# Performance work log

Measured on AMD Instinct MI355X. Metric: run time of the kernel, lower is better.

Reference implementation:

```python
import jax, jax.numpy as jnp
import numpy as np

K = 16  # neighbors


def knn(x, k):
    # x: [B,N,C]; returns indices of k nearest points (incl. self) [B,N,k]
    sq = jnp.sum(x * x, axis=-1)
    d = sq[:, :, None] + sq[:, None, :] - 2.0 * jnp.einsum('bnc,bmc->bnm', x, x)
    return jax.lax.top_k(-d, k)[1]


def gather_nbrs(x, idx):
    # x: [B,N,C], idx: [B,N,k] -> [B,N,k,C]
    return jax.vmap(lambda xb, ib: xb[ib])(x, idx)


def bn(x, g, b, m, v):
    # Keras BatchNormalization inference mode, eps=1e-3
    return (x - m) * g * jax.lax.rsqrt(v + 1e-3) + b


def dense(x, w, b):
    # Conv1D(kernel_size=1) == pointwise dense over channels
    return jnp.einsum('bnc,co->bno', x, w) + b


def graph_layer(h, k, lw, lb, cw, cb, relu_out):
    g = gather_nbrs(h, knn(h, k))          # [B,N,k,C]
    m = jnp.max(g, axis=2)                 # [B,N,C] max over neighbors
    m = dense(dense(m, lw, lb), cw, cb)
    return jax.nn.relu(m) if relu_out else m


def setup_inputs():
    key = jax.random.key(0)
    ks = jax.random.split(key, 16)
    B, N = 16, 2048
    inp = {'x': jax.random.normal(ks[0], (B, N, 3), jnp.float32)}
    dims = [('conv1', 12, 12), ('conv2', 12, 64), ('conv3', 64, 64),
            ('g1_lin', 64, 64), ('g1_conv', 64, 128),
            ('g2_lin', 128, 128), ('g2_conv', 128, 1024),
            ('conv4', 1024, 1024), ('conv5', 1024, 512)]
    for j, (name, i, o) in enumerate(dims):
        s = (2.0 / (i + o)) ** 0.5  # glorot-ish
        inp[name + '_w'] = jax.random.normal(ks[j + 1], (i, o), jnp.float32) * s
        inp[name + '_b'] = jnp.zeros((o,), jnp.float32)
    for name, c in [('bn1', 12), ('bn2', 64), ('bn3', 64)]:
        inp[name + '_g'] = jnp.ones((c,), jnp.float32)
        inp[name + '_b'] = jnp.zeros((c,), jnp.float32)
        inp[name + '_m'] = jnp.zeros((c,), jnp.float32)
        inp[name + '_v'] = jnp.ones((c,), jnp.float32)
    return inp


def reference(x, conv1_w, conv1_b, conv2_w, conv2_b, conv3_w, conv3_b,
              g1_lin_w, g1_lin_b, g1_conv_w, g1_conv_b,
              g2_lin_w, g2_lin_b, g2_conv_w, g2_conv_b,
              conv4_w, conv4_b, conv5_w, conv5_b,
              bn1_g, bn1_b, bn1_m, bn1_v,
              bn2_g, bn2_b, bn2_m, bn2_v,
              bn3_g, bn3_b, bn3_m, bn3_v):
    B, N = x.shape[0], x.shape[1]
    kx = gather_nbrs(x, knn(x, K))                        # [B,N,K,3]
    c = kx - jnp.mean(kx, axis=2, keepdims=True)
    cov = jnp.einsum('bnki,bnkj->bnij', c, c)             # [B,N,3,3]
    h = jnp.concatenate([x, cov.reshape(B, N, 9)], axis=2)  # [B,N,12]
    h = jax.nn.relu(bn(dense(h, conv1_w, conv1_b), bn1_g, bn1_b, bn1_m, bn1_v))
    h = jax.nn.relu(bn(dense(h, conv2_w, conv2_b), bn2_g, bn2_b, bn2_m, bn2_v))
    h = jax.nn.relu(bn(dense(h, conv3_w, conv3_b), bn3_g, bn3_b, bn3_m, bn3_v))
    h = graph_layer(h, K, g1_lin_w, g1_lin_b, g1_conv_w, g1_conv_b, True)    # [B,N,128]
    h = graph_layer(h, K, g2_lin_w, g2_lin_b, g2_conv_w, g2_conv_b, False)   # [B,N,1024]
    h = jnp.max(h, axis=1, keepdims=True)                 # [B,1,1024]
    h = jax.nn.relu(dense(h, conv4_w, conv4_b))
    return dense(h, conv5_w, conv5_b)                     # [B,1,512]
```

## Files before the change

### kernel.cpp

```cpp
#include <hip/hip_runtime.h>
#include <cstddef>
#include <cstdint>

#define NPTS 2048

typedef short bf16x8 __attribute__((ext_vector_type(8)));
typedef float f32x4 __attribute__((ext_vector_type(4)));

__device__ __forceinline__ unsigned short f2bf(float f) {
  unsigned u = __builtin_bit_cast(unsigned, f);
  unsigned r = u + 0x7fffu + ((u >> 16) & 1u);
  return (unsigned short)(r >> 16);
}
__device__ __forceinline__ float bf2f(unsigned short s) {
  unsigned u = ((unsigned)s) << 16;
  return __builtin_bit_cast(float, u);
}
__device__ __forceinline__ unsigned f2sort(float f) {
  unsigned u = __builtin_bit_cast(unsigned, f);
  return u ^ (unsigned)(((int)u >> 31) | 0x80000000);
}

__device__ __forceinline__ void pool_insert(uint64_t k, uint64_t& s0, uint64_t& s1,
                                            uint64_t& s2, uint64_t& s3) {
  s3 = k < s3 ? k : s3;
  uint64_t t;
  t = s2 < s3 ? s2 : s3; s3 = s2 < s3 ? s3 : s2; s2 = t;
  t = s1 < s2 ? s1 : s2; s2 = s1 < s2 ? s2 : s1; s1 = t;
  t = s0 < s1 ? s0 : s1; s1 = s0 < s1 ? s1 : s0; s0 = t;
}

__device__ __forceinline__ int mbcnt64(unsigned long long m) {
  return __builtin_amdgcn_mbcnt_hi((unsigned)(m >> 32),
                                   __builtin_amdgcn_mbcnt_lo((unsigned)m, 0));
}

__device__ __forceinline__ float wave_sum_f32(float v) {
#pragma unroll
  for (int s = 1; s < 64; s <<= 1) v += __shfl_xor(v, s, 64);
  return v;
}

__global__ __launch_bounds__(256) void k_knn1_cov(const float* __restrict__ x,
                                                  float* __restrict__ h0) {
  const int b = blockIdx.y;
  const int tid = threadIdx.x;
  const int lane = tid & 63;
  const int w = tid >> 6;
  __shared__ float4 xsq[NPTS];
  const float* xb = x + (size_t)b * NPTS * 3;
  for (int i = tid; i < NPTS; i += 256) {
    float a0 = xb[3 * i], a1 = xb[3 * i + 1], a2 = xb[3 * i + 2];
    xsq[i] = make_float4(a0, a1, a2, fmaf(a0, a0, fmaf(a1, a1, a2 * a2)));
  }
  __syncthreads();
  const int nq = blockIdx.x * 4 + w;
  const float4 q4 = xsq[nq];
  const float sqq = q4.w;
  float d[32];
  uint64_t s0 = ~0ull, s1 = ~0ull, s2 = ~0ull, s3 = ~0ull;
#pragma unroll
  for (int j = 0; j < 32; ++j) {
    float4 v = xsq[j * 64 + lane];
    float dot = q4.x * v.x;
    dot = fmaf(q4.y, v.y, dot);
    dot = fmaf(q4.z, v.z, dot);
    float dd = fmaf(-2.f, dot, sqq + v.w);
    d[j] = dd;
    uint64_t k = ((uint64_t)f2sort(dd) << 32) | (unsigned)(j * 64 + lane);
    pool_insert(k, s0, s1, s2, s3);
  }
  const unsigned h0w = (unsigned)(s0 >> 32), m0i = (unsigned)s0;
  const unsigned h1w = (unsigned)(s1 >> 32), m1i = (unsigned)s1;
  const unsigned h2w = (unsigned)(s2 >> 32), m2i = (unsigned)s2;
  const unsigned h3w = (unsigned)(s3 >> 32), m3i = (unsigned)s3;
  unsigned H = 0;
#pragma unroll 1
  for (int bit = 31; bit >= 0; --bit) {
    unsigned tr = H | (1u << bit);
    int c = __popcll(__ballot(h0w < tr)) + __popcll(__ballot(h1w < tr)) +
            __popcll(__ballot(h2w < tr)) + __popcll(__ballot(h3w < tr));
    if (c < 16) H = tr;
  }
  const int cs = __popcll(__ballot(h0w < H)) + __popcll(__ballot(h1w < H)) +
                 __popcll(__ballot(h2w < H)) + __popcll(__ballot(h3w < H));
  const int rneed = 16 - cs;
  const bool e0 = (h0w == H), e1 = (h1w == H), e2 = (h2w == H), e3 = (h3w == H);
  const int gsz = __popcll(__ballot(e0)) + __popcll(__ballot(e1)) +
                  __popcll(__ballot(e2)) + __popcll(__ballot(e3));
  unsigned I = 0xFFFFFFFFu;
  if (gsz > rneed) {
    unsigned Iv = 0;
#pragma unroll 1
    for (int bit = 10; bit >= 0; --bit) {
      unsigned tr = Iv | (1u << bit);
      int c2 = __popcll(__ballot(e0 && m0i < tr)) + __popcll(__ballot(e1 && m1i < tr)) +
               __popcll(__ballot(e2 && m2i < tr)) + __popcll(__ballot(e3 && m3i < tr));
      if (c2 < rneed) Iv = tr;
    }
    I = Iv;
  }
  const bool sel0 = (h0w < H) | (e0 & (m0i <= I));
  const bool sel1 = (h1w < H) | (e1 & (m1i <= I));
  const bool sel2 = (h2w < H) | (e2 & (m2i <= I));
  const bool sel3 = (h3w < H) | (e3 & (m3i <= I));
  const int nsel = (int)sel0 + sel1 + sel2 + sel3;
  float cxx, cxy, cxz, cyy, cyz, czz;
  if (__ballot(nsel == 4) == 0ull) {
    float4 z = make_float4(0.f, 0.f, 0.f, 0.f);
    float4 v0 = sel0 ? xsq[m0i] : z;
    float4 v1 = sel1 ? xsq[m1i] : z;
    float4 v2 = sel2 ? xsq[m2i] : z;
    float4 v3 = sel3 ? xsq[m3i] : z;
    float sx = wave_sum_f32(v0.x + v1.x + v2.x + v3.x);
    float sy = wave_sum_f32(v0.y + v1.y + v2.y + v3.y);
    float sz = wave_sum_f32(v0.z + v1.z + v2.z + v3.z);
    const float mx = sx * 0.0625f, my = sy * 0.0625f, mz = sz * 0.0625f;
    float w0 = sel0 ? 1.f : 0.f, w1 = sel1 ? 1.f : 0.f;
    float w2 = sel2 ? 1.f : 0.f, w3 = sel3 ? 1.f : 0.f;
    float a0x = v0.x - mx, a0y = v0.y - my, a0z = v0.z - mz;
    float a1x = v1.x - mx, a1y = v1.y - my, a1z = v1.z - mz;
    float a2x = v2.x - mx, a2y = v2.y - my, a2z = v2.z - mz;
    float a3x = v3.x - mx, a3y = v3.y - my, a3z = v3.z - mz;
    float pxx = (w0 * a0x) * a0x + (w1 * a1x) * a1x + (w2 * a2x) * a2x + (w3 * a3x) * a3x;
    float pxy = (w0 * a0x) * a0y + (w1 * a1x) * a1y + (w2 * a2x) * a2y + (w3 * a3x) * a3y;
    float pxz = (w0 * a0x) * a0z + (w1 * a1x) * a1z + (w2 * a2x) * a2z + (w3 * a3x) * a3z;
    float pyy = (w0 * a0y) * a0y + (w1 * a1y) * a1y + (w2 * a2y) * a2y + (w3 * a3y) * a3y;
    float pyz = (w0 * a0y) * a0z + (w1 * a1y) * a1z + (w2 * a2y) * a2z + (w3 * a3y) * a3z;
    float pzz = (w0 * a0z) * a0z + (w1 * a1z) * a1z + (w2 * a2z) * a2z + (w3 * a3z) * a3z;
    cxx = wave_sum_f32(pxx); cxy = wave_sum_f32(pxy); cxz = wave_sum_f32(pxz);
    cyy = wave_sum_f32(pyy); cyz = wave_sum_f32(pyz); czz = wave_sum_f32(pzz);
  } else {
    unsigned mask = 0;
    int widx[16];
#pragma unroll 1
    for (int r = 0; r < 16; ++r) {
      float vmin = 3.4e38f;
      int mmin = 0x7fffffff;
#pragma unroll
      for (int j = 0; j < 32; ++j) {
        bool ok = !((mask >> j) & 1u) && (d[j] < vmin);
        if (ok) { vmin = d[j]; mmin = j * 64 + lane; }
      }
#pragma unroll
      for (int s = 1; s < 64; s <<= 1) {
        float ov = __shfl_xor(vmin, s, 64);
        int om = __shfl_xor(mmin, s, 64);
        if (ov < vmin || (ov == vmin && om < mmin)) { vmin = ov; mmin = om; }
      }
      widx[r] = mmin;
      if (lane == (mmin & 63)) mask |= 1u << (mmin >> 6);
    }
    float sx = 0, sy = 0, sz = 0;
#pragma unroll
    for (int r = 0; r < 16; ++r) {
      float4 v = xsq[widx[r]];
      sx += v.x; sy += v.y; sz += v.z;
    }
    const float mx = sx * 0.0625f, my = sy * 0.0625f, mz = sz * 0.0625f;
    cxx = cxy = cxz = cyy = cyz = czz = 0.f;
#pragma unroll
    for (int r = 0; r < 16; ++r) {
      float4 v = xsq[widx[r]];
      float ax = v.x - mx, ay = v.y - my, az = v.z - mz;
      cxx = fmaf(ax, ax, cxx); cxy = fmaf(ax, ay, cxy); cxz = fmaf(ax, az, cxz);
      cyy = fmaf(ay, ay, cyy); cyz = fmaf(ay, az, cyz); czz = fmaf(az, az, czz);
    }
  }
  if (lane == 0) {
    float* o = h0 + ((size_t)b * NPTS + nq) * 12;
    *(float4*)&o[0] = make_float4(q4.x, q4.y, q4.z, cxx);
    *(float4*)&o[4] = make_float4(cxy, cxz, cxy, cyy);
    *(float4*)&o[8] = make_float4(cyz, cxz, cyz, czz);
  }
}

__global__ __launch_bounds__(256) void k_mlp1(
    const float* __restrict__ h0,
    const float* __restrict__ w1, const float* __restrict__ cb1,
    const float* __restrict__ w2, const float* __restrict__ cb2,
    const float* __restrict__ w3, const float* __restrict__ cb3,
    const float* __restrict__ bn1g, const float* __restrict__ bn1b,
    const float* __restrict__ bn1m, const float* __restrict__ bn1v,
    const float* __restrict__ bn2g, const float* __restrict__ bn2b,
    const float* __restrict__ bn2m, const float* __restrict__ bn2v,
    const float* __restrict__ bn3g, const float* __restrict__ bn3b,
    const float* __restrict__ bn3m, const float* __restrict__ bn3v,
    float* __restrict__ h3out,
    unsigned short* __restrict__ h3hi, unsigned short* __restrict__ h3lo) {
  __shared__ float W1[144], W2[768], W3[4096];
  __shared__ float S1[12], F1[12], S2[64], F2[64], S3[64], F3[64];
  __shared__ float h0s[64][12];
  __shared__ float A2[64][65];
  const int tid = threadIdx.x;
  for (int i = tid; i < 144; i += 256) W1[i] = w1[i];
  for (int i = tid; i < 768; i += 256) W2[i] = w2[i];
  for (int i = tid; i < 4096; i += 256) W3[i] = w3[i];
  if (tid < 12) {
    float s = bn1g[tid] * rsqrtf(bn1v[tid] + 1e-3f);
    S1[tid] = s; F1[tid] = (cb1[tid] - bn1m[tid]) * s + bn1b[tid];
  }
  if (tid < 64) {
    float s2 = bn2g[tid] * rsqrtf(bn2v[tid] + 1e-3f);
    S2[tid] = s2; F2[tid] = (cb2[tid] - bn2m[tid]) * s2 + bn2b[tid];
    float s3 = bn3g[tid] * rsqrtf(bn3v[tid] + 1e-3f);
    S3[tid] = s3; F3[tid] = (cb3[tid] - bn3m[tid]) * s3 + bn3b[tid];
  }
  const int p0 = blockIdx.x * 64;
  for (int i = tid; i < 64 * 12; i += 256)
    h0s[i / 12][i % 12] = h0[(size_t)p0 * 12 + i];
  __syncthreads();
  const int pl = tid >> 2;
  const int q = tid & 3;
  float v1[12];
#pragma unroll
  for (int o = 0; o < 12; ++o) {
    float a = 0.f;
#pragma unroll
    for (int i = 0; i < 12; ++i) a = fmaf(h0s[pl][i], W1[i * 12 + o], a);
    v1[o] = fmaxf(fmaf(a, S1[o], F1[o]), 0.f);
  }
#pragma unroll
  for (int o = 0; o < 16; ++o) {
    int oo = q * 16 + o;
    float a = 0.f;
#pragma unroll
    for (int i = 0; i < 12; ++i) a = fmaf(v1[i], W2[i * 64 + oo], a);
    A2[pl][oo] = fmaxf(fmaf(a, S2[oo], F2[oo]), 0.f);
  }
  __syncthreads();
  float acc[16];
#pragma unroll
  for (int o = 0; o < 16; ++o) acc[o] = 0.f;
  for (int i = 0; i < 64; ++i) {
    float xv = A2[pl][i];
#pragma unroll
    for (int o = 0; o < 16; ++o) acc[o] = fmaf(xv, W3[i * 64 + q * 16 + o], acc[o]);
  }
  float vals[16];
#pragma unroll
  for (int o = 0; o < 16; ++o) {
    int oo = q * 16 + o;
    vals[o] = fmaxf(fmaf(acc[o], S3[oo], F3[oo]), 0.f);
  }
  const size_t rowo = (size_t)(p0 + pl) * 64 + q * 16;
  float* orow = h3out + rowo;
#pragma unroll
  for (int o4 = 0; o4 < 4; ++o4)
    *(float4*)&orow[4 * o4] = make_float4(vals[4 * o4], vals[4 * o4 + 1],
                                          vals[4 * o4 + 2], vals[4 * o4 + 3]);
  bf16x8 hv0, hv1, lv0, lv1;
#pragma unroll
  for (int o = 0; o < 8; ++o) {
    unsigned short hb = f2bf(vals[o]);
    hv0[o] = (short)hb; lv0[o] = (short)f2bf(vals[o] - bf2f(hb));
    unsigned short hb1 = f2bf(vals[8 + o]);
    hv1[o] = (short)hb1; lv1[o] = (short)f2bf(vals[8 + o] - bf2f(hb1));
  }
  *(bf16x8*)&h3hi[rowo] = hv0; *(bf16x8*)&h3hi[rowo + 8] = hv1;
  *(bf16x8*)&h3lo[rowo] = lv0; *(bf16x8*)&h3lo[rowo + 8] = lv1;
}

template <int C>
__global__ __launch_bounds__(256) void k_sqnorm(const float* __restrict__ h,
                                                float* __restrict__ sq) {
  const int p = blockIdx.x * 256 + threadIdx.x;
  const float* row = h + (size_t)p * C;
  float a = 0.f;
#pragma unroll
  for (int i = 0; i < C; ++i) a = fmaf(row[i], row[i], a);
  sq[p] = a;
}

#define DSTRIDE 2052
template <int C>
__global__ __launch_bounds__(1024, 4) void k_knn_fused(
    const unsigned short* __restrict__ hi, const unsigned short* __restrict__ lo,
    const float* __restrict__ sq, const float* __restrict__ h,
    unsigned short* __restrict__ mhi, unsigned short* __restrict__ mlo) {
  __shared__ float dmat[16][DSTRIDE];
  __shared__ unsigned nidx[16][16];
  const int tid = threadIdx.x, lane = tid & 63, w = tid >> 6;
  const int f = blockIdx.x;
  const int g = ((f & 7) << 8) | (f >> 3);
  const int b = g >> 7;
  const int q0 = (g & 127) * 16;
  const size_t base = (size_t)b * NPTS * C;
  const float* __restrict__ sqb = sq + (size_t)b * NPTS;
  const int r = lane & 15, ks = (lane >> 4) * 8;
  const unsigned short* Ah = hi + base + (size_t)(q0 + r) * C + ks;
  const unsigned short* Al = lo + base + (size_t)(q0 + r) * C + ks;
  float sqq[4];
#pragma unroll
  for (int r2 = 0; r2 < 4; ++r2) sqq[r2] = sqb[q0 + (lane >> 4) * 4 + r2];

  {
    const int m0 = w * 128;
    const unsigned short* Bh = hi + base + (size_t)(m0 + r) * C + ks;
    const unsigned short* Bl = lo + base + (size_t)(m0 + r) * C + ks;
    f32x4 acc[8];
#pragma unroll
    for (int s = 0; s < 8; ++s) acc[s] = (f32x4){0.f, 0.f, 0.f, 0.f};
#pragma unroll
    for (int kk = 0; kk < C; kk += 32) {
      bf16x8 ah = *(const bf16x8*)(Ah + kk);
      bf16x8 al = *(const bf16x8*)(Al + kk);
#pragma unroll
      for (int s = 0; s < 8; ++s) {
        bf16x8 bh = *(const bf16x8*)(Bh + (size_t)s * 16 * C + kk);
        bf16x8 bl = *(const bf16x8*)(Bl + (size_t)s * 16 * C + kk);
        acc[s] = __builtin_amdgcn_mfma_f32_16x16x32_bf16(ah, bh, acc[s], 0, 0, 0);
        acc[s] = __builtin_amdgcn_mfma_f32_16x16x32_bf16(ah, bl, acc[s], 0, 0, 0);
        acc[s] = __builtin_amdgcn_mfma_f32_16x16x32_bf16(al, bh, acc[s], 0, 0, 0);
      }
    }
#pragma unroll
    for (int s = 0; s < 8; ++s) {
      const int col = m0 + s * 16 + (lane & 15);
      float smc = sqb[col];
#pragma unroll
      for (int r2 = 0; r2 < 4; ++r2)
        dmat[(lane >> 4) * 4 + r2][col] = fmaf(-2.f, acc[s][r2], sqq[r2] + smc);
    }
  }
  __syncthreads();

  const float* __restrict__ hbp = h + base;
  const int q = q0 + w;
  uint64_t s0 = ~0ull, s1 = ~0ull, s2 = ~0ull, s3 = ~0ull;
#pragma unroll
  for (int t = 0; t < 8; ++t) {
    float4 dv = *(const float4*)&dmat[w][t * 256 + 4 * lane];
    const unsigned mb = (unsigned)(t * 256 + 4 * lane);
    pool_insert(((uint64_t)f2sort(dv.x) << 32) | (mb + 0), s0, s1, s2, s3);
    pool_insert(((uint64_t)f2sort(dv.y) << 32) | (mb + 1), s0, s1, s2, s3);
    pool_insert(((uint64_t)f2sort(dv.z) << 32) | (mb + 2), s0, s1, s2, s3);
    pool_insert(((uint64_t)f2sort(dv.w) << 32) | (mb + 3), s0, s1, s2, s3);
  }
  const unsigned h0 = (unsigned)(s0 >> 32), m0i = (unsigned)s0;
  const unsigned h1 = (unsigned)(s1 >> 32), m1i = (unsigned)s1;
  const unsigned h2 = (unsigned)(s2 >> 32), m2i = (unsigned)s2;
  const unsigned h3 = (unsigned)(s3 >> 32), m3i = (unsigned)s3;
  unsigned H = 0;
#pragma unroll 1
  for (int bit = 31; bit >= 0; --bit) {
    unsigned tr = H | (1u << bit);
    int c = __popcll(__ballot(h0 < tr)) + __popcll(__ballot(h1 < tr)) +
            __popcll(__ballot(h2 < tr)) + __popcll(__ballot(h3 < tr));
    if (c < 16) H = tr;
  }
  const int cs = __popcll(__ballot(h0 < H)) + __popcll(__ballot(h1 < H)) +
                 __popcll(__ballot(h2 < H)) + __popcll(__ballot(h3 < H));
  const int rneed = 16 - cs;
  const bool e0 = (h0 == H), e1 = (h1 == H), e2 = (h2 == H), e3 = (h3 == H);
  const int gsz = __popcll(__ballot(e0)) + __popcll(__ballot(e1)) +
                  __popcll(__ballot(e2)) + __popcll(__ballot(e3));
  unsigned I = 0xFFFFFFFFu;
  if (gsz > rneed) {
    unsigned Iv = 0;
#pragma unroll 1
    for (int bit = 10; bit >= 0; --bit) {
      unsigned tr = Iv | (1u << bit);
      int c2 = __popcll(__ballot(e0 && m0i < tr)) + __popcll(__ballot(e1 && m1i < tr)) +
               __popcll(__ballot(e2 && m2i < tr)) + __popcll(__ballot(e3 && m3i < tr));
      if (c2 < rneed) Iv = tr;
    }
    I = Iv;
  }
  const bool sel0 = (h0 < H) | (e0 & (m0i <= I));
  const bool sel1 = (h1 < H) | (e1 & (m1i <= I));
  const bool sel2 = (h2 < H) | (e2 & (m2i <= I));
  const bool sel3 = (h3 < H) | (e3 & (m3i <= I));
  const int nsel = (int)sel0 + sel1 + sel2 + sel3;
  float g0 = -3.4e38f, g1 = -3.4e38f;
  if (__ballot(nsel == 4) == 0ull) {
    unsigned long long bm;
    int bpos = 0;
    bm = __ballot(sel0); if (sel0) nidx[w][bpos + mbcnt64(bm)] = m0i; bpos += __popcll(bm);
    bm = __ballot(sel1); if (sel1) nidx[w][bpos + mbcnt64(bm)] = m1i; bpos += __popcll(bm);
    bm = __ballot(sel2); if (sel2) nidx[w][bpos + mbcnt64(bm)] = m2i; bpos += __popcll(bm);
    bm = __ballot(sel3); if (sel3) nidx[w][bpos + mbcnt64(bm)] = m3i;
#pragma unroll
    for (int rr = 0; rr < 16; ++rr) {
      unsigned m = nidx[w][rr];
      const float* row = hbp + (size_t)m * C;
      g0 = fmaxf(g0, row[lane]);
      if (C == 128) g1 = fmaxf(g1, row[64 + lane]);
    }
  } else {
    unsigned mask = 0u;
#pragma unroll 1
    for (int rr = 0; rr < 16; ++rr) {
      float vmin = 3.4e38f;
      int mmin = 0x7fffffff;
#pragma unroll
      for (int j = 0; j < 32; ++j) {
        const int m = (j >> 2) * 256 + 4 * lane + (j & 3);
        float dj = dmat[w][m];
        bool ok = !((mask >> j) & 1u) && (dj < vmin);
        if (ok) { vmin = dj; mmin = m; }
      }
#pragma unroll
      for (int s = 1; s < 64; s <<= 1) {
        float ov = __shfl_xor(vmin, s, 64);
        int om = __shfl_xor(mmin, s, 64);
        if (ov < vmin || (ov == vmin && om < mmin)) { vmin = ov; mmin = om; }
      }
      if (lane == ((mmin >> 2) & 63)) mask |= 1u << (((mmin >> 8) << 2) | (mmin & 3));
      const float* row = hbp + (size_t)mmin * C;
      g0 = fmaxf(g0, row[lane]);
      if (C == 128) g1 = fmaxf(g1, row[64 + lane]);
    }
  }
  const size_t orow = base + (size_t)q * C;
  unsigned short h0b = f2bf(g0);
  mhi[orow + lane] = h0b;
  mlo[orow + lane] = f2bf(g0 - bf2f(h0b));
  if (C == 128) {
    unsigned short h1b = f2bf(g1);
    mhi[orow + 64 + lane] = h1b;
    mlo[orow + 64 + lane] = f2bf(g1 - bf2f(h1b));
  }
}

__global__ __launch_bounds__(256) void k_combine_t(const float* __restrict__ lw,
                                                   const float* __restrict__ lb,
                                                   const float* __restrict__ cw,
                                                   const float* __restrict__ cb,
                                                   unsigned short* __restrict__ wthi,
                                                   unsigned short* __restrict__ wtlo,
                                                   float* __restrict__ bc, int K, int M) {
  const int id = blockIdx.x * 256 + threadIdx.x;
  if (id < K * M) {
    int i = id / M, o = id % M;
    float a = 0.f;
    for (int k = 0; k < K; ++k) a = fmaf(lw[i * K + k], cw[k * M + o], a);
    unsigned short hb = f2bf(a);
    wthi[(size_t)o * K + i] = hb;
    wtlo[(size_t)o * K + i] = f2bf(a - bf2f(hb));
  }
  if (id < M) {
    float a = cb[id];
    for (int k = 0; k < K; ++k) a = fmaf(lb[k], cw[k * M + id], a);
    bc[id] = a;
  }
}

template <int K, int M>
__global__ __launch_bounds__(256) void k_apply_relu(
    const unsigned short* __restrict__ Ah, const unsigned short* __restrict__ Al,
    const unsigned short* __restrict__ Wh, const unsigned short* __restrict__ Wl,
    const float* __restrict__ bias, float* __restrict__ fout,
    unsigned short* __restrict__ phi, unsigned short* __restrict__ plo) {
  const int tid = threadIdx.x, lane = tid & 63, w = tid >> 6;
  const int q0 = blockIdx.x * 64 + w * 16;
  const int m0 = blockIdx.y * 128;
  const int r = lane & 15, ks = (lane >> 4) * 8;
  const unsigned short* ap_h = Ah + (size_t)(q0 + r) * K + ks;
  const unsigned short* ap_l = Al + (size_t)(q0 + r) * K + ks;
  const unsigned short* bp_h = Wh + (size_t)(m0 + r) * K + ks;
  const unsigned short* bp_l = Wl + (size_t)(m0 + r) * K + ks;
  f32x4 acc[8];
#pragma unroll
  for (int mt = 0; mt < 8; ++mt) acc[mt] = (f32x4){0.f, 0.f, 0.f, 0.f};
#pragma unroll
  for (int kk = 0; kk < K; kk += 32) {
    bf16x8 ah = *(const bf16x8*)(ap_h + kk);
    bf16x8 al = *(const bf16x8*)(ap_l + kk);
#pragma unroll
    for (int mt = 0; mt < 8; ++mt) {
      bf16x8 bh = *(const bf16x8*)(bp_h + (size_t)mt * 16 * K + kk);
      bf16x8 bl = *(const bf16x8*)(bp_l + (size_t)mt * 16 * K + kk);
      acc[mt] = __builtin_amdgcn_mfma_f32_16x16x32_bf16(ah, bh, acc[mt], 0, 0, 0);
      acc[mt] = __builtin_amdgcn_mfma_f32_16x16x32_bf16(ah, bl, acc[mt], 0, 0, 0);
      acc[mt] = __builtin_amdgcn_mfma_f32_16x16x32_bf16(al, bh, acc[mt], 0, 0, 0);
    }
  }
#pragma unroll
  for (int mt = 0; mt < 8; ++mt) {
    const int col = m0 + mt * 16 + (lane & 15);
    const float bv = bias[col];
#pragma unroll
    for (int r2 = 0; r2 < 4; ++r2) {
      const int row = q0 + (lane >> 4) * 4 + r2;
      float v = fmaxf(acc[mt][r2] + bv, 0.f);
      const size_t idx = (size_t)row * M + col;
      fout[idx] = v;
      unsigned short hb = f2bf(v);
      phi[idx] = hb;
      plo[idx] = f2bf(v - bf2f(hb));
    }
  }
}

#define WSTRIDE 136
__global__ __launch_bounds__(256, 2) void k_apply_colmax(
    const unsigned short* __restrict__ Ah, const unsigned short* __restrict__ Al,
    const unsigned short* __restrict__ Wh, const unsigned short* __restrict__ Wl,
    const float* __restrict__ bias, float* __restrict__ P) {
  constexpr int K = 128, M = 1024;
  __shared__ unsigned short Bh_s[128 * WSTRIDE];
  __shared__ unsigned short Bl_s[128 * WSTRIDE];
  __shared__ float cm[4][128];
  const int tid = threadIdx.x, lane = tid & 63, w = tid >> 6;
  const int rblk = blockIdx.x;
  const int m0 = blockIdx.y * 128;
  const int r = lane & 15, ks = (lane >> 4) * 8;
  for (int i = tid; i < 128 * 16; i += 256) {
    int row = i >> 4, c8 = (i & 15) * 8;
    *(bf16x8*)&Bh_s[row * WSTRIDE + c8] = *(const bf16x8*)&Wh[(size_t)(m0 + row) * K + c8];
    *(bf16x8*)&Bl_s[row * WSTRIDE + c8] = *(const bf16x8*)&Wl[(size_t)(m0 + row) * K + c8];
  }
  __syncthreads();
  const int q0 = rblk * 256 + w * 64;
  f32x4 acc[4][8];
#pragma unroll
  for (int st = 0; st < 4; ++st)
#pragma unroll
    for (int mt = 0; mt < 8; ++mt) acc[st][mt] = (f32x4){0.f, 0.f, 0.f, 0.f};
#pragma unroll
  for (int kk = 0; kk < K; kk += 32) {
    bf16x8 bh[8], bl[8];
#pragma unroll
    for (int mt = 0; mt < 8; ++mt) {
      bh[mt] = *(const bf16x8*)&Bh_s[(mt * 16 + r) * WSTRIDE + ks + kk];
      bl[mt] = *(const bf16x8*)&Bl_s[(mt * 16 + r) * WSTRIDE + ks + kk];
    }
#pragma unroll
    for (int st = 0; st < 4; ++st) {
      const unsigned short* ap_h = Ah + (size_t)(q0 + st * 16 + r) * K + ks + kk;
      const unsigned short* ap_l = Al + (size_t)(q0 + st * 16 + r) * K + ks + kk;
      bf16x8 ah = *(const bf16x8*)ap_h;
      bf16x8 al = *(const bf16x8*)ap_l;
#pragma unroll
      for (int mt = 0; mt < 8; ++mt) {
        acc[st][mt] = __builtin_amdgcn_mfma_f32_16x16x32_bf16(ah, bh[mt], acc[st][mt], 0, 0, 0);
        acc[st][mt] = __builtin_amdgcn_mfma_f32_16x16x32_bf16(ah, bl[mt], acc[st][mt], 0, 0, 0);
        acc[st][mt] = __builtin_amdgcn_mfma_f32_16x16x32_bf16(al, bh[mt], acc[st][mt], 0, 0, 0);
      }
    }
  }
#pragma unroll
  for (int mt = 0; mt < 8; ++mt) {
    float v = -3.4e38f;
#pragma unroll
    for (int st = 0; st < 4; ++st) {
      v = fmaxf(v, fmaxf(fmaxf(acc[st][mt][0], acc[st][mt][1]),
                         fmaxf(acc[st][mt][2], acc[st][mt][3])));
    }
    v = fmaxf(v, __shfl_xor(v, 16, 64));
    v = fmaxf(v, __shfl_xor(v, 32, 64));
    cm[w][mt * 16 + (lane & 15)] = v;
  }
  __syncthreads();
  if (tid < 128) {
    float m = fmaxf(fmaxf(cm[0][tid], cm[1][tid]), fmaxf(cm[2][tid], cm[3][tid]));
    P[(size_t)rblk * M + m0 + tid] = m + bias[m0 + tid];
  }
}

__global__ __launch_bounds__(256) void k_reduce_max(const float* __restrict__ P,
                                                    float* __restrict__ gmax) {
  const int b = blockIdx.x, tid = threadIdx.x;
  for (int c = tid; c < 1024; c += 256) {
    float m = P[(size_t)(b * 8) * 1024 + c];
    for (int rt = 1; rt < 8; ++rt)
      m = fmaxf(m, P[(size_t)(b * 8 + rt) * 1024 + c]);
    gmax[b * 1024 + c] = m;
  }
}

__global__ __launch_bounds__(256) void k_head1(const float* __restrict__ gmax,
                                               const float* __restrict__ w4,
                                               const float* __restrict__ b4,
                                               float* __restrict__ hid) {
  const int b = blockIdx.y, c0 = blockIdx.x * 64;
  const int tid = threadIdx.x;
  const int c = tid & 63, iq = tid >> 6;
  __shared__ float xs[1024];
  __shared__ float red[4][64];
  for (int i = tid; i < 1024; i += 256) xs[i] = gmax[b * 1024 + i];
  __syncthreads();
  float a = 0.f;
  for (int i = iq * 256; i < iq * 256 + 256; ++i)
    a = fmaf(xs[i], w4[(size_t)i * 1024 + c0 + c], a);
  red[iq][c] = a;
  __syncthreads();
  if (tid < 64) {
    float v = red[0][tid] + red[1][tid] + red[2][tid] + red[3][tid];
    hid[b * 1024 + c0 + tid] = fmaxf(v + b4[c0 + tid], 0.f);
  }
}

__global__ __launch_bounds__(256) void k_head2(const float* __restrict__ hid,
                                               const float* __restrict__ w5,
                                               const float* __restrict__ b5,
                                               float* __restrict__ out) {
  const int b = blockIdx.y, c0 = blockIdx.x * 64;
  const int tid = threadIdx.x;
  const int c = tid & 63, iq = tid >> 6;
  __shared__ float xs[1024];
  __shared__ float red[4][64];
  for (int i = tid; i < 1024; i += 256) xs[i] = hid[b * 1024 + i];
  __syncthreads();
  float a = 0.f;
  for (int i = iq * 256; i < iq * 256 + 256; ++i)
    a = fmaf(xs[i], w5[(size_t)i * 512 + c0 + c], a);
  red[iq][c] = a;
  __syncthreads();
  if (tid < 64) {
    float v = red[0][tid] + red[1][tid] + red[2][tid] + red[3][tid];
    out[(size_t)b * 512 + c0 + tid] = v + b5[c0 + tid];
  }
}

extern "C" void kernel_launch(void* const* d_in, const int* in_sizes, int n_in,
                              void* d_out, int out_size, void* d_ws, size_t ws_size,
                              hipStream_t stream) {
  (void)in_sizes; (void)n_in; (void)out_size; (void)ws_size;
  const float* x = (const float*)d_in[0];
  const float* w1 = (const float*)d_in[1];  const float* b1 = (const float*)d_in[2];
  const float* w2 = (const float*)d_in[3];  const float* b2 = (const float*)d_in[4];
  const float* w3 = (const float*)d_in[5];  const float* b3 = (const float*)d_in[6];
  const float* g1lw = (const float*)d_in[7];  const float* g1lb = (const float*)d_in[8];
  const float* g1cw = (const float*)d_in[9];  const float* g1cb = (const float*)d_in[10];
  const float* g2lw = (const float*)d_in[11]; const float* g2lb = (const float*)d_in[12];
  const float* g2cw = (const float*)d_in[13]; const float* g2cb = (const float*)d_in[14];
  const float* w4 = (const float*)d_in[15]; const float* b4 = (const float*)d_in[16];
  const float* w5 = (const float*)d_in[17]; const float* b5 = (const float*)d_in[18];
  const float* bn1g = (const float*)d_in[19]; const float* bn1b = (const float*)d_in[20];
  const float* bn1m = (const float*)d_in[21]; const float* bn1v = (const float*)d_in[22];
  const float* bn2g = (const float*)d_in[23]; const float* bn2b = (const float*)d_in[24];
  const float* bn2m = (const float*)d_in[25]; const float* bn2v = (const float*)d_in[26];
  const float* bn3g = (const float*)d_in[27]; const float* bn3b = (const float*)d_in[28];
  const float* bn3m = (const float*)d_in[29]; const float* bn3v = (const float*)d_in[30];

  float* ws = (float*)d_ws;
  size_t off = 0;
  auto alloc = [&](size_t n) { float* p = ws + off; off += (n + 63) & ~(size_t)63; return p; };
  float* slotA = alloc(16u * 2048 * 128);
  float* slotB = alloc(16u * 2048 * 64);
  float* sqv  = alloc(16u * 2048);
  unsigned short* hi_h = (unsigned short*)alloc(16u * 2048 * 64);
  unsigned short* lo_h = (unsigned short*)alloc(16u * 2048 * 64);
  unsigned short* mhi = (unsigned short*)alloc(16u * 2048 * 64);
  unsigned short* mlo = (unsigned short*)alloc(16u * 2048 * 64);
  unsigned short* wthi = (unsigned short*)alloc(65536);
  unsigned short* wtlo = (unsigned short*)alloc(65536);
  float* bc   = alloc(1024);
  float* P    = alloc(128u * 1024);
  float* gm   = alloc(16u * 1024);
  float* hid  = alloc(16u * 1024);

  k_knn1_cov<<<dim3(512, 16), 256, 0, stream>>>(x, slotA);
  k_mlp1<<<512, 256, 0, stream>>>(slotA, w1, b1, w2, b2, w3, b3,
                                  bn1g, bn1b, bn1m, bn1v,
                                  bn2g, bn2b, bn2m, bn2v,
                                  bn3g, bn3b, bn3m, bn3v, slotB, hi_h, lo_h);
  k_sqnorm<64><<<128, 256, 0, stream>>>(slotB, sqv);
  k_knn_fused<64><<<2048, 1024, 0, stream>>>(hi_h, lo_h, sqv, slotB, mhi, mlo);
  k_combine_t<<<32, 256, 0, stream>>>(g1lw, g1lb, g1cw, g1cb, wthi, wtlo, bc, 64, 128);
  k_apply_relu<64, 128><<<dim3(512, 1), 256, 0, stream>>>(
      mhi, mlo, wthi, wtlo, bc, slotA, hi_h, lo_h);
  k_sqnorm<128><<<128, 256, 0, stream>>>(slotA, sqv);
  k_knn_fused<128><<<2048, 1024, 0, stream>>>(hi_h, lo_h, sqv, slotA, mhi, mlo);
  k_combine_t<<<512, 256, 0, stream>>>(g2lw, g2lb, g2cw, g2cb, wthi, wtlo, bc, 128, 1024);
  k_apply_colmax<<<dim3(128, 8), 256, 0, stream>>>(mhi, mlo, wthi, wtlo, bc, P);
  k_reduce_max<<<16, 256, 0, stream>>>(P, gm);
  k_head1<<<dim3(16, 16), 256, 0, stream>>>(gm, w4, b4, hid);
  k_head2<<<dim3(8, 16), 256, 0, stream>>>(hid, w5, b5, (float*)d_out);
}
```

Before: 890.3 us.

## Add register-resident streaming kNN pool kernel with fallback for overflowed lanes

Adds a new kNN kernel that computes distance tiles with MFMA and streams them through per-lane sorted top-8 register pools (two pools per query across 4 lane groups), then merges them with wave shuffles to get the top 16 and max-pools the neighbor features directly. When any pool may have dropped a true neighbor (a pool contributed all 8 entries), the query is flagged and the original shared-memory kNN kernel recomputes that block. This avoids materializing the 16x2048 distance matrix in LDS and the full-row selection for most blocks. In exchange it adds an extra launch, a flags buffer, and a per-block early-exit check, and the fallback's cost depends on how often pools overflow.

```diff
diff --git a/kernel.cpp b/kernel.cpp
--- a/kernel.cpp
+++ b/kernel.cpp
@@ -39,6 +39,22 @@
 #pragma unroll
   for (int s = 1; s < 64; s <<= 1) v += __shfl_xor(v, s, 64);
   return v;
+}
+
+__device__ __forceinline__ void ins8(unsigned ku, unsigned ii,
+                                     unsigned (&kd)[8], unsigned (&pi)[8]) {
+  bool c = ku < kd[7];
+  kd[7] = c ? ku : kd[7];
+  pi[7] = c ? ii : pi[7];
+#pragma unroll
+  for (int i = 6; i >= 0; --i) {
+    bool s = kd[i + 1] < kd[i];
+    unsigned tk = s ? kd[i + 1] : kd[i];
+    unsigned tp = s ? pi[i + 1] : pi[i];
+    kd[i + 1] = s ? kd[i] : kd[i + 1];
+    pi[i + 1] = s ? pi[i] : pi[i + 1];
+    kd[i] = tk; pi[i] = tp;
+  }
 }
 
 __global__ __launch_bounds__(256) void k_knn1_cov(const float* __restrict__ x,
@@ -272,19 +288,148 @@
   sq[p] = a;
 }
 
+template <int C>
+__global__ __launch_bounds__(256, 2) void k_knn_pool(
+    const unsigned short* __restrict__ hi, const unsigned short* __restrict__ lo,
+    const float* __restrict__ sq, const float* __restrict__ h,
+    unsigned short* __restrict__ mhi, unsigned short* __restrict__ mlo,
+    int* __restrict__ flags) {
+  constexpr int KK = C / 32;
+  constexpr int DL = C / 4;
+  const int tid = threadIdx.x, lane = tid & 63, w = tid >> 6;
+  const int f = blockIdx.x;
+  const int g = ((f & 7) << 6) | (f >> 3);
+  const int b = g >> 5;
+  const int q0 = ((g & 31) * 4 + w) * 16;
+  const size_t base = (size_t)b * NPTS * C;
+  const float* __restrict__ sqb = sq + (size_t)b * NPTS;
+  const int r = lane & 15, g4 = lane >> 4, ks = g4 * 8;
+  bf16x8 bh[KK], bl[KK];
+#pragma unroll
+  for (int k4 = 0; k4 < KK; ++k4) {
+    bh[k4] = *(const bf16x8*)&hi[base + (size_t)(q0 + r) * C + k4 * 32 + ks];
+    bl[k4] = *(const bf16x8*)&lo[base + (size_t)(q0 + r) * C + k4 * 32 + ks];
+  }
+  const float sqq = sqb[q0 + r];
+  unsigned kdA[8], piA[8], kdB[8], piB[8];
+#pragma unroll
+  for (int i = 0; i < 8; ++i) {
+    kdA[i] = 0xFFFFFFFFu; piA[i] = 0xFFFFFFFFu;
+    kdB[i] = 0xFFFFFFFFu; piB[i] = 0xFFFFFFFFu;
+  }
+#pragma unroll 1
+  for (int t = 0; t < 128; ++t) {
+    f32x4 acc = (f32x4){0.f, 0.f, 0.f, 0.f};
+    const unsigned short* ap_h = hi + base + (size_t)(t * 16 + r) * C + ks;
+    const unsigned short* ap_l = lo + base + (size_t)(t * 16 + r) * C + ks;
+#pragma unroll
+    for (int k4 = 0; k4 < KK; ++k4) {
+      bf16x8 ah = *(const bf16x8*)(ap_h + k4 * 32);
+      bf16x8 al = *(const bf16x8*)(ap_l + k4 * 32);
+      acc = __builtin_amdgcn_mfma_f32_16x16x32_bf16(ah, bh[k4], acc, 0, 0, 0);
+      acc = __builtin_amdgcn_mfma_f32_16x16x32_bf16(al, bh[k4], acc, 0, 0, 0);
+      acc = __builtin_amdgcn_mfma_f32_16x16x32_bf16(ah, bl[k4], acc, 0, 0, 0);
+    }
+    float4 sqc = *(const float4*)&sqb[t * 16 + g4 * 4];
+    const unsigned ib = (unsigned)(t * 16 + g4 * 4);
+    {
+      float dd = fmaf(-2.f, acc[0], sqq + sqc.x);
+      ins8(f2sort(dd), ib + 0, kdA, piA);
+    }
+    {
+      float dd = fmaf(-2.f, acc[1], sqq + sqc.y);
+      ins8(f2sort(dd), ib + 1, kdB, piB);
+    }
+    {
+      float dd = fmaf(-2.f, acc[2], sqq + sqc.z);
+      ins8(f2sort(dd), ib + 2, kdA, piA);
+    }
+    {
+      float dd = fmaf(-2.f, acc[3], sqq + sqc.w);
+      ins8(f2sort(dd), ib + 3, kdB, piB);
+    }
+  }
+  const float* __restrict__ hbp = h + base;
+  int cntA = 0, cntB = 0;
+  float gm[DL];
+#pragma unroll
+  for (int j = 0; j < DL; ++j) gm[j] = -3.4e38f;
+#pragma unroll 1
+  for (int rr = 0; rr < 16; ++rr) {
+    uint64_t kA = ((uint64_t)kdA[0] << 32) | piA[0];
+    uint64_t kB = ((uint64_t)kdB[0] << 32) | piB[0];
+    uint64_t kc = kA < kB ? kA : kB;
+    uint64_t km = kc;
+    uint64_t o1 = __shfl_xor((unsigned long long)km, 16, 64);
+    km = o1 < km ? o1 : km;
+    o1 = __shfl_xor((unsigned long long)km, 32, 64);
+    km = o1 < km ? o1 : km;
+    const bool exA = (kA == km);
+    const bool exB = (kB == km);
+    cntA += exA ? 1 : 0;
+    cntB += exB ? 1 : 0;
+#pragma unroll
+    for (int i = 0; i < 7; ++i) {
+      kdA[i] = exA ? kdA[i + 1] : kdA[i]; piA[i] = exA ? piA[i + 1] : piA[i];
+      kdB[i] = exB ? kdB[i + 1] : kdB[i]; piB[i] = exB ? piB[i + 1] : piB[i];
+    }
+    kdA[7] = exA ? 0xFFFFFFFFu : kdA[7]; piA[7] = exA ? 0xFFFFFFFFu : piA[7];
+    kdB[7] = exB ? 0xFFFFFFFFu : kdB[7]; piB[7] = exB ? 0xFFFFFFFFu : piB[7];
+    const unsigned m = (unsigned)km;
+    const float* row = hbp + (size_t)m * C + g4 * DL;
+#pragma unroll
+    for (int j4 = 0; j4 < DL / 4; ++j4) {
+      float4 v = *(const float4*)&row[j4 * 4];
+      gm[j4 * 4 + 0] = fmaxf(gm[j4 * 4 + 0], v.x);
+      gm[j4 * 4 + 1] = fmaxf(gm[j4 * 4 + 1], v.y);
+      gm[j4 * 4 + 2] = fmaxf(gm[j4 * 4 + 2], v.z);
+      gm[j4 * 4 + 3] = fmaxf(gm[j4 * 4 + 3], v.w);
+    }
+  }
+  const bool of = (cntA == 8) || (cntB == 8);
+  unsigned long long bal = __ballot(of);
+  unsigned qm = (unsigned)((bal >> r) | (bal >> (r + 16)) | (bal >> (r + 32)) |
+                           (bal >> (r + 48)));
+  if (g4 == 0) flags[b * NPTS + q0 + r] = (int)(qm & 1u);
+  const size_t orow = base + (size_t)(q0 + r) * C + g4 * DL;
+#pragma unroll
+  for (int j8 = 0; j8 < DL / 8; ++j8) {
+    bf16x8 hv, lv;
+#pragma unroll
+    for (int jj = 0; jj < 8; ++jj) {
+      float v = gm[j8 * 8 + jj];
+      unsigned short hb = f2bf(v);
+      hv[jj] = (short)hb;
+      lv[jj] = (short)f2bf(v - bf2f(hb));
+    }
+    *(bf16x8*)&mhi[orow + j8 * 8] = hv;
+    *(bf16x8*)&mlo[orow + j8 * 8] = lv;
+  }
+}
+
 #define DSTRIDE 2052
 template <int C>
 __global__ __launch_bounds__(1024, 4) void k_knn_fused(
     const unsigned short* __restrict__ hi, const unsigned short* __restrict__ lo,
     const float* __restrict__ sq, const float* __restrict__ h,
-    unsigned short* __restrict__ mhi, unsigned short* __restrict__ mlo) {
+    unsigned short* __restrict__ mhi, unsigned short* __restrict__ mlo,
+    const int* __restrict__ flags) {
   __shared__ float dmat[16][DSTRIDE];
   __shared__ unsigned nidx[16][16];
+  __shared__ int anyf;
   const int tid = threadIdx.x, lane = tid & 63, w = tid >> 6;
   const int f = blockIdx.x;
   const int g = ((f & 7) << 8) | (f >> 3);
   const int b = g >> 7;
   const int q0 = (g & 127) * 16;
+  if (tid == 0) {
+    int s = 0;
+#pragma unroll 1
+    for (int i = 0; i < 16; ++i) s |= flags[b * NPTS + q0 + i];
+    anyf = s;
+  }
+  __syncthreads();
+  if (!anyf) return;
   const size_t base = (size_t)b * NPTS * C;
   const float* __restrict__ sqb = sq + (size_t)b * NPTS;
   const int r = lane & 15, ks = (lane >> 4) * 8;
@@ -293,7 +438,6 @@
   float sqq[4];
 #pragma unroll
   for (int r2 = 0; r2 < 4; ++r2) sqq[r2] = sqb[q0 + (lane >> 4) * 4 + r2];
-
   {
     const int m0 = w * 128;
     const unsigned short* Bh = hi + base + (size_t)(m0 + r) * C + ks;
@@ -307,11 +451,11 @@
       bf16x8 al = *(const bf16x8*)(Al + kk);
 #pragma unroll
       for (int s = 0; s < 8; ++s) {
-        bf16x8 bh = *(const bf16x8*)(Bh + (size_t)s * 16 * C + kk);
-        bf16x8 bl = *(const bf16x8*)(Bl + (size_t)s * 16 * C + kk);
-        acc[s] = __builtin_amdgcn_mfma_f32_16x16x32_bf16(ah, bh, acc[s], 0, 0, 0);
-        acc[s] = __builtin_amdgcn_mfma_f32_16x16x32_bf16(ah, bl, acc[s], 0, 0, 0);
-        acc[s] = __builtin_amdgcn_mfma_f32_16x16x32_bf16(al, bh, acc[s], 0, 0, 0);
+        bf16x8 bhv = *(const bf16x8*)(Bh + (size_t)s * 16 * C + kk);
+        bf16x8 blv = *(const bf16x8*)(Bl + (size_t)s * 16 * C + kk);
+        acc[s] = __builtin_amdgcn_mfma_f32_16x16x32_bf16(ah, bhv, acc[s], 0, 0, 0);
+        acc[s] = __builtin_amdgcn_mfma_f32_16x16x32_bf16(ah, blv, acc[s], 0, 0, 0);
+        acc[s] = __builtin_amdgcn_mfma_f32_16x16x32_bf16(al, bhv, acc[s], 0, 0, 0);
       }
     }
 #pragma unroll
@@ -324,7 +468,6 @@
     }
   }
   __syncthreads();
-
   const float* __restrict__ hbp = h + base;
   const int q = q0 + w;
   uint64_t s0 = ~0ull, s1 = ~0ull, s2 = ~0ull, s3 = ~0ull;
@@ -651,6 +794,7 @@
   float* P    = alloc(128u * 1024);
   float* gm   = alloc(16u * 1024);
   float* hid  = alloc(16u * 1024);
+  int* flags  = (int*)alloc(16u * 2048);
 
   k_knn1_cov<<<dim3(512, 16), 256, 0, stream>>>(x, slotA);
   k_mlp1<<<512, 256, 0, stream>>>(slotA, w1, b1, w2, b2, w3, b3,
@@ -658,12 +802,14 @@
                                   bn2g, bn2b, bn2m, bn2v,
                                   bn3g, bn3b, bn3m, bn3v, slotB, hi_h, lo_h);
   k_sqnorm<64><<<128, 256, 0, stream>>>(slotB, sqv);
-  k_knn_fused<64><<<2048, 1024, 0, stream>>>(hi_h, lo_h, sqv, slotB, mhi, mlo);
+  k_knn_pool<64><<<512, 256, 0, stream>>>(hi_h, lo_h, sqv, slotB, mhi, mlo, flags);
+  k_knn_fused<64><<<2048, 1024, 0, stream>>>(hi_h, lo_h, sqv, slotB, mhi, mlo, flags);
   k_combine_t<<<32, 256, 0, stream>>>(g1lw, g1lb, g1cw, g1cb, wthi, wtlo, bc, 64, 128);
   k_apply_relu<64, 128><<<dim3(512, 1), 256, 0, stream>>>(
       mhi, mlo, wthi, wtlo, bc, slotA, hi_h, lo_h);
   k_sqnorm<128><<<128, 256, 0, stream>>>(slotA, sqv);
-  k_knn_fused<128><<<2048, 1024, 0, stream>>>(hi_h, lo_h, sqv, slotA, mhi, mlo);
+  k_knn_pool<128><<<512, 256, 0, stream>>>(hi_h, lo_h, sqv, slotA, mhi, mlo, flags);
+  k_knn_fused<128><<<2048, 1024, 0, stream>>>(hi_h, lo_h, sqv, slotA, mhi, mlo, flags);
   k_combine_t<<<512, 256, 0, stream>>>(g2lw, g2lb, g2cw, g2cb, wthi, wtlo, bc, 128, 1024);
   k_apply_colmax<<<dim3(128, 8), 256, 0, stream>>>(mhi, mlo, wthi, wtlo, bc, P);
   k_reduce_max<<<16, 256, 0, stream>>>(P, gm);
```

After: 815.7 us (median of 2 runs). 1.09x faster.
